# Kernel optimization log

Measured on AMD Instinct MI355X. Metric: run time of the kernel, lower is better.

## Reference

```python
import jax, jax.numpy as jnp
import numpy as np

NEG_BIG = -1e4  # matches torch masked_fill(-1e4)


def word_average(hidden, word_ids, num_words):
    """Segment-mean of token embeddings into word embeddings.
    hidden: [M, L, D], word_ids: [M, L] int in [0, num_words).
    Returns (word_reprs [M, W, D], word_mask [M, W] bool).
    Equivalent to average_by_spans: each word repr is the mean of its subword tokens;
    words with no tokens (the torch code's skipped [-1] spans) get a zero repr and mask=0.
    """
    M, L, D = hidden.shape
    seg = (jnp.arange(M, dtype=word_ids.dtype)[:, None] * num_words + word_ids).reshape(-1)
    sums = jax.ops.segment_sum(hidden.reshape(M * L, D), seg, num_segments=M * num_words)
    counts = jax.ops.segment_sum(jnp.ones((M * L,), hidden.dtype), seg, num_segments=M * num_words)
    sums = sums.reshape(M, num_words, D)
    counts = counts.reshape(M, num_words)
    mask = counts > 0
    reprs = sums / jnp.maximum(counts, 1.0)[..., None]
    return reprs, mask


def scope_pool(word_reprs, mask, proj_w, proj_b, scope_importance):
    """scope_proj_head (eval-mode dropout = identity) + scope_aware_pooling.
    word_reprs: [M, W, D], mask: [M, W]. Returns (pooled [M, D], logits [M, W, S]).
    Logits at invalid (padded) word slots are zeroed, matching torch pad_sequence padding
    applied after the projection.
    """
    logits = (jnp.einsum('mwd,ds->mws', word_reprs, proj_w) + proj_b) * mask[..., None].astype(word_reprs.dtype)
    scope_probs = jax.nn.softmax(logits, axis=-1)                      # [M, W, S]
    importance = jnp.einsum('mws,s->mw', scope_probs, scope_importance)
    importance = jnp.where(mask, importance, NEG_BIG)
    weights = jax.nn.softmax(importance, axis=-1)                      # [M, W]
    pooled = jnp.einsum('mw,mwd->md', weights, word_reprs)             # [M, D]
    return pooled, logits


def setup_inputs() -> dict:
    key = jax.random.key(0)
    ks = jax.random.split(key, 9)
    B, N, Lq, Lp, D, S = 16, 7, 256, 512, 768, 12
    Wq, Wp = 200, 400
    return {
        'q_hidden': jax.random.normal(ks[0], (B, Lq, D), jnp.float32),
        'pos_hidden': jax.random.normal(ks[1], (B, Lp, D), jnp.float32),
        'neg_hidden': jax.random.normal(ks[2], (B, N, Lp, D), jnp.float32),
        'proj_w': jax.random.normal(ks[3], (D, S), jnp.float32) * 0.02,
        'proj_b': jax.random.normal(ks[4], (S,), jnp.float32) * 0.02,
        'scope_importance': jax.random.uniform(ks[5], (S,), jnp.float32),
        'q_word_ids': jax.random.randint(ks[6], (B, Lq), 0, Wq, jnp.int32),
        'pos_word_ids': jax.random.randint(ks[7], (B, Lp), 0, Wp, jnp.int32),
        'neg_word_ids': jax.random.randint(ks[8], (B, N, Lp), 0, Wp, jnp.int32),
    }


def reference(q_hidden, pos_hidden, neg_hidden, proj_w, proj_b, scope_importance,
              q_word_ids, pos_word_ids, neg_word_ids):
    Wq = 200
    Wp = 400
    B, N, Lp, D = neg_hidden.shape

    # per-sample span averaging (ragged segment means)
    q_word, q_mask = word_average(q_hidden, q_word_ids, Wq)
    p_word, p_mask = word_average(pos_hidden, pos_word_ids, Wp)
    n_word, n_mask = word_average(neg_hidden.reshape(B * N, Lp, D),
                                  neg_word_ids.reshape(B * N, Lp), Wp)

    # scope projection + scope-aware softmax pooling
    q_pooled, q_logits = scope_pool(q_word, q_mask, proj_w, proj_b, scope_importance)
    p_pooled, p_logits = scope_pool(p_word, p_mask, proj_w, proj_b, scope_importance)
    n_pooled, _ = scope_pool(n_word, n_mask, proj_w, proj_b, scope_importance)
    n_pooled = n_pooled.reshape(B, N, D)

    return q_pooled, p_pooled, q_logits, p_logits, n_pooled
```

## Files before the change

kernel.cpp:

```cpp
#include <hip/hip_runtime.h>
#include <cfloat>

#define NEG_BIG (-1e4f)

constexpr int D = 768;
constexpr int S = 12;

constexpr int Lq = 256, Lp = 512, Wq = 200, Wp = 400;
constexpr int Mq = 16, Mp = 16, Mn = 112;

constexpr int OFF_WSUM_Q = 0;
constexpr int OFF_WSUM_P = 38400;
constexpr int OFF_WSUM_N = 115200;
constexpr int OFF_CNT_Q  = 652800;
constexpr int OFF_CNT_P  = 656000;
constexpr int OFF_CNT_N  = 662400;
constexpr int OFF_IMP_Q  = 707200;
constexpr int OFF_IMP_P  = 710400;
constexpr int OFF_IMP_N  = 716800;
constexpr int OFF_COEF   = 761600;
constexpr int WS_ZERO_FLOATS = 707200;

constexpr int OUT_QP = 0;
constexpr int OUT_PP = 12288;
constexpr int OUT_QL = 24576;
constexpr int OUT_PL = 62976;
constexpr int OUT_NP = 139776;

__global__ __launch_bounds__(192) void k_proj_accum(
    const float* __restrict__ q_h, const float* __restrict__ p_h,
    const float* __restrict__ n_h, const int* __restrict__ q_ids,
    const int* __restrict__ p_ids, const int* __restrict__ n_ids,
    const float* __restrict__ pw, float* __restrict__ ws)
{
    const int bx   = blockIdx.x;
    const int lane = threadIdx.x & 63;
    const int wv   = threadIdx.x >> 6;

    const float* h; const int* ids; float* wsum; float* cnt;
    int L, W, m, t0;
    if (bx < 128)      { h = q_h; ids = q_ids; wsum = ws + OFF_WSUM_Q; cnt = ws + OFF_CNT_Q;
                         L = Lq; W = Wq; m = bx >> 3;  t0 = (bx & 7) * 32; }
    else if (bx < 384) { int r = bx - 128;
                         h = p_h; ids = p_ids; wsum = ws + OFF_WSUM_P; cnt = ws + OFF_CNT_P;
                         L = Lp; W = Wp; m = r >> 4;  t0 = (r & 15) * 32; }
    else               { int r = bx - 384;
                         h = n_h; ids = n_ids; wsum = ws + OFF_WSUM_N; cnt = ws + OFF_CNT_N;
                         L = Lp; W = Wp; m = r >> 4;  t0 = (r & 15) * 32; }

    const int d0 = 256 * wv + 4 * lane;
    float wreg[4][S];
    {
        const float4* base = (const float4*)(pw + (size_t)d0 * S);
#pragma unroll
        for (int q = 0; q < 12; ++q) {
            float4 v = base[q];
            float tmp[4] = {v.x, v.y, v.z, v.w};
#pragma unroll
            for (int c = 0; c < 4; ++c) {
                const int li = 4 * q + c;
                wreg[li / 12][li % 12] = tmp[c];
            }
        }
    }

    const float* hbase = h + (size_t)m * L * D + d0;
    const int*   idrow = ids + m * L;

    const bool b5 = lane & 32, b4 = lane & 16, b3 = lane & 8, b2 = lane & 4;
    const int  off_s = b3 ? 2 : (b2 ? 1 : 0);
    const int  s_fin = (b5 ? 6 : 0) + (b4 ? 3 : 0) + off_s;
    const bool do_at = ((lane & 3) == 0) && !(b3 && b2);

#pragma unroll 4
    for (int t = t0; t < t0 + 32; ++t) {
        const int id = idrow[t];
        const float4 hv = *(const float4*)(hbase + (size_t)t * D);

        float p[S];
        {
            const float hj[4] = {hv.x, hv.y, hv.z, hv.w};
#pragma unroll
            for (int s = 0; s < S; ++s) p[s] = hj[0] * wreg[0][s];
#pragma unroll
            for (int j = 1; j < 4; ++j)
#pragma unroll
                for (int s = 0; s < S; ++s)
                    p[s] = fmaf(hj[j], wreg[j][s], p[s]);
        }

        float a[6];
#pragma unroll
        for (int i = 0; i < 6; ++i) {
            float snd = b5 ? p[i] : p[6 + i];
            float kp  = b5 ? p[6 + i] : p[i];
            a[i] = kp + __shfl_xor(snd, 32, 64);
        }
        float b[3];
#pragma unroll
        for (int i = 0; i < 3; ++i) {
            float snd = b4 ? a[i] : a[3 + i];
            float kp  = b4 ? a[3 + i] : a[i];
            b[i] = kp + __shfl_xor(snd, 16, 64);
        }
        float c0, c1;
        {
            float snd0 = b3 ? b[0] : b[2];
            float kp0  = b3 ? b[2] : b[0];
            c0 = kp0 + __shfl_xor(snd0, 8, 64);
            float snd1 = b3 ? b[1] : 0.f;
            float kp1  = b3 ? 0.f  : b[1];
            c1 = kp1 + __shfl_xor(snd1, 8, 64);
        }
        float snd = b3 ? c0 : (b2 ? c0 : c1);
        float kp  = b3 ? c0 : (b2 ? c1 : c0);
        float d   = kp + __shfl_xor(snd, 4, 64);
        d += __shfl_xor(d, 2, 64);
        d += __shfl_xor(d, 1, 64);

        float* wb = wsum + ((size_t)m * W + id) * S;
        if (do_at)                atomicAdd(wb + s_fin, d);
        if (wv == 0 && lane == 1) atomicAdd(cnt + (size_t)m * W + id, 1.0f);
    }
}

__global__ void k_finalize(
    const float* __restrict__ ws_c, float* __restrict__ ws_mut,
    const float* __restrict__ pb, const float* __restrict__ simp,
    float* __restrict__ out)
{
    const int idx = blockIdx.x * blockDim.x + threadIdx.x;
    if (idx >= Mq * Wq + Mp * Wp + Mn * Wp) return;

    const float* wsum; float c; float* imp; float* lgout;
    if (idx < Mq * Wq) {
        wsum = ws_c + OFF_WSUM_Q + (size_t)idx * S;  c = ws_c[OFF_CNT_Q + idx];
        imp = ws_mut + OFF_IMP_Q + idx;              lgout = out + OUT_QL + (size_t)idx * S;
    } else if (idx < Mq * Wq + Mp * Wp) {
        const int r = idx - Mq * Wq;
        wsum = ws_c + OFF_WSUM_P + (size_t)r * S;    c = ws_c[OFF_CNT_P + r];
        imp = ws_mut + OFF_IMP_P + r;                lgout = out + OUT_PL + (size_t)r * S;
    } else {
        const int r = idx - Mq * Wq - Mp * Wp;
        wsum = ws_c + OFF_WSUM_N + (size_t)r * S;    c = ws_c[OFF_CNT_N + r];
        imp = ws_mut + OFF_IMP_N + r;                lgout = nullptr;
    }

    const bool valid = (c > 0.5f);
    const float inv = valid ? 1.0f / c : 0.0f;

    float lg[S];
#pragma unroll
    for (int s = 0; s < S; ++s)
        lg[s] = valid ? (wsum[s] * inv + pb[s]) : 0.0f;

    float mx = lg[0];
#pragma unroll
    for (int s = 1; s < S; ++s) mx = fmaxf(mx, lg[s]);
    float sum = 0.f, acc = 0.f;
#pragma unroll
    for (int s = 0; s < S; ++s) {
        float e = expf(lg[s] - mx);
        sum += e;
        acc += e * simp[s];
    }
    *imp = valid ? (acc / sum) : NEG_BIG;

    if (lgout) {
#pragma unroll
        for (int s = 0; s < S; ++s) lgout[s] = lg[s];
    }
}

__global__ __launch_bounds__(256) void k_coef(
    const int* __restrict__ q_ids, const int* __restrict__ p_ids,
    const int* __restrict__ n_ids, float* __restrict__ ws)
{
    __shared__ float s_red[256];
    __shared__ float s_wgt[Wp];

    const int by  = blockIdx.x;
    const int tid = threadIdx.x;

    const int* ids; const float* impm; const float* cntm; int L, W;
    if (by < Mq)           { int m = by;
        ids = q_ids + m * Lq; impm = ws + OFF_IMP_Q + m * Wq;
        cntm = ws + OFF_CNT_Q + m * Wq; L = Lq; W = Wq; }
    else if (by < Mq + Mp) { int m = by - Mq;
        ids = p_ids + m * Lp; impm = ws + OFF_IMP_P + m * Wp;
        cntm = ws + OFF_CNT_P + m * Wp; L = Lp; W = Wp; }
    else                   { int m = by - Mq - Mp;
        ids = n_ids + m * Lp; impm = ws + OFF_IMP_N + m * Wp;
        cntm = ws + OFF_CNT_N + m * Wp; L = Lp; W = Wp; }
    float* coef = ws + OFF_COEF + (size_t)by * 512;

    float lm = -FLT_MAX;
    for (int w = tid; w < W; w += 256) lm = fmaxf(lm, impm[w]);
    s_red[tid] = lm;
    __syncthreads();
    for (int st = 128; st > 0; st >>= 1) {
        if (tid < st) s_red[tid] = fmaxf(s_red[tid], s_red[tid + st]);
        __syncthreads();
    }
    const float mx = s_red[0];
    __syncthreads();

    float ls = 0.f;
    for (int w = tid; w < W; w += 256) {
        float e = expf(impm[w] - mx);
        s_wgt[w] = e;
        ls += e;
    }
    s_red[tid] = ls;
    __syncthreads();
    for (int st = 128; st > 0; st >>= 1) {
        if (tid < st) s_red[tid] += s_red[tid + st];
        __syncthreads();
    }
    const float inv = 1.0f / s_red[0];
    for (int w = tid; w < W; w += 256) s_wgt[w] *= inv;
    __syncthreads();

    for (int l = tid; l < L; l += 256) {
        const int id = ids[l];
        coef[l] = s_wgt[id] / cntm[id];
    }
}

__global__ __launch_bounds__(192) void k_pool(
    const float* __restrict__ q_h, const float* __restrict__ p_h,
    const float* __restrict__ n_h, const float* __restrict__ ws,
    float* __restrict__ out)
{
    __shared__ float s_c[64];

    const int bx  = blockIdx.x;
    const int tid = threadIdx.x;

    const float* h; float* outp; int L, m, t0, cby;
    if (bx < 64)       { m = bx >> 2;  t0 = (bx & 3) * 64;
        h = q_h; outp = out + OUT_QP + (size_t)m * D; L = Lq; cby = m; }
    else if (bx < 192) { int r = bx - 64;  m = r >> 3;  t0 = (r & 7) * 64;
        h = p_h; outp = out + OUT_PP + (size_t)m * D; L = Lp; cby = Mq + m; }
    else               { int r = bx - 192; m = r >> 3;  t0 = (r & 7) * 64;
        h = n_h; outp = out + OUT_NP + (size_t)m * D; L = Lp; cby = Mq + Mp + m; }

    if (tid < 64) s_c[tid] = ws[OFF_COEF + (size_t)cby * 512 + t0 + tid];
    __syncthreads();

    const float* hb = h + (size_t)m * L * D + (size_t)t0 * D + 4 * tid;

    float4 acc = make_float4(0.f, 0.f, 0.f, 0.f);
#pragma unroll 8
    for (int l = 0; l < 64; ++l) {
        const float4 hv = *(const float4*)(hb + (size_t)l * D);
        const float c = s_c[l];
        acc.x = fmaf(c, hv.x, acc.x);
        acc.y = fmaf(c, hv.y, acc.y);
        acc.z = fmaf(c, hv.z, acc.z);
        acc.w = fmaf(c, hv.w, acc.w);
    }

    float* op = outp + 4 * tid;
    atomicAdd(op + 0, acc.x);
    atomicAdd(op + 1, acc.y);
    atomicAdd(op + 2, acc.z);
    atomicAdd(op + 3, acc.w);
}

extern "C" void kernel_launch(void* const* d_in, const int* in_sizes, int n_in,
                              void* d_out, int out_size, void* d_ws, size_t ws_size,
                              hipStream_t stream)
{
    const float* q_hidden   = (const float*)d_in[0];
    const float* pos_hidden = (const float*)d_in[1];
    const float* neg_hidden = (const float*)d_in[2];
    const float* proj_w     = (const float*)d_in[3];
    const float* proj_b     = (const float*)d_in[4];
    const float* simp       = (const float*)d_in[5];
    const int*   q_ids      = (const int*)d_in[6];
    const int*   p_ids      = (const int*)d_in[7];
    const int*   n_ids      = (const int*)d_in[8];
    float* out = (float*)d_out;
    float* ws  = (float*)d_ws;

    hipMemsetAsync(d_ws, 0, (size_t)WS_ZERO_FLOATS * sizeof(float), stream);
    hipMemsetAsync(out, 0, (size_t)24576 * sizeof(float), stream);
    hipMemsetAsync(out + OUT_NP, 0, (size_t)(Mn * D) * sizeof(float), stream);

    k_proj_accum<<<dim3(2176), dim3(192), 0, stream>>>(
        q_hidden, pos_hidden, neg_hidden, q_ids, p_ids, n_ids, proj_w, ws);

    k_finalize<<<dim3((Mq * Wq + Mp * Wp + Mn * Wp + 255) / 256), dim3(256), 0, stream>>>(
        ws, ws, proj_b, simp, out);

    k_coef<<<dim3(Mq + Mp + Mn), dim3(256), 0, stream>>>(q_ids, p_ids, n_ids, ws);

    k_pool<<<dim3(1088), dim3(192), 0, stream>>>(
        q_hidden, pos_hidden, neg_hidden, ws, out);
}
```

Measured before the change: 357.6 us.

## Assign one token per thread in projection kernel, drop cross-lane shuffle reduction

The projection-accumulate kernel now gives each thread one token and half of the hidden dimension (384 values), and accumulates all 12 scope logits in registers. This replaces the old mapping, in which each wave split D across lanes and needed a shuffle-tree reduction for every token. The change removes the shuffle work and issues 12 atomics per thread per token-half. In exchange, each lane reads a separate 3KB row, so global loads become strided and uncoalesced across lanes. Projection weights now come from memory (broadcast across the wave) instead of registers, and blocks shrink from 192 to 64 threads.

```diff
diff --git a/kernel.cpp b/kernel.cpp
--- a/kernel.cpp
+++ b/kernel.cpp
@@ -27,101 +27,54 @@
 constexpr int OUT_PL = 62976;
 constexpr int OUT_NP = 139776;
 
-__global__ __launch_bounds__(192) void k_proj_accum(
+__global__ __launch_bounds__(64) void k_proj_accum(
     const float* __restrict__ q_h, const float* __restrict__ p_h,
     const float* __restrict__ n_h, const int* __restrict__ q_ids,
     const int* __restrict__ p_ids, const int* __restrict__ n_ids,
     const float* __restrict__ pw, float* __restrict__ ws)
 {
     const int bx   = blockIdx.x;
-    const int lane = threadIdx.x & 63;
-    const int wv   = threadIdx.x >> 6;
+    const int lane = threadIdx.x;
 
     const float* h; const int* ids; float* wsum; float* cnt;
-    int L, W, m, t0;
+    int W, Lshift, tile, half;
     if (bx < 128)      { h = q_h; ids = q_ids; wsum = ws + OFF_WSUM_Q; cnt = ws + OFF_CNT_Q;
-                         L = Lq; W = Wq; m = bx >> 3;  t0 = (bx & 7) * 32; }
+                         W = Wq; Lshift = 8; tile = bx >> 1; half = bx & 1; }
     else if (bx < 384) { int r = bx - 128;
                          h = p_h; ids = p_ids; wsum = ws + OFF_WSUM_P; cnt = ws + OFF_CNT_P;
-                         L = Lp; W = Wp; m = r >> 4;  t0 = (r & 15) * 32; }
+                         W = Wp; Lshift = 9; tile = r >> 1; half = r & 1; }
     else               { int r = bx - 384;
                          h = n_h; ids = n_ids; wsum = ws + OFF_WSUM_N; cnt = ws + OFF_CNT_N;
-                         L = Lp; W = Wp; m = r >> 4;  t0 = (r & 15) * 32; }
-
-    const int d0 = 256 * wv + 4 * lane;
-    float wreg[4][S];
-    {
-        const float4* base = (const float4*)(pw + (size_t)d0 * S);
-#pragma unroll
-        for (int q = 0; q < 12; ++q) {
-            float4 v = base[q];
-            float tmp[4] = {v.x, v.y, v.z, v.w};
-#pragma unroll
-            for (int c = 0; c < 4; ++c) {
-                const int li = 4 * q + c;
-                wreg[li / 12][li % 12] = tmp[c];
-            }
-        }
-    }
-
-    const float* hbase = h + (size_t)m * L * D + d0;
-    const int*   idrow = ids + m * L;
-
-    const bool b5 = lane & 32, b4 = lane & 16, b3 = lane & 8, b2 = lane & 4;
-    const int  off_s = b3 ? 2 : (b2 ? 1 : 0);
-    const int  s_fin = (b5 ? 6 : 0) + (b4 ? 3 : 0) + off_s;
-    const bool do_at = ((lane & 3) == 0) && !(b3 && b2);
+                         W = Wp; Lshift = 9; tile = r >> 1; half = r & 1; }
+
+    const int flat = tile * 64 + lane;
+    const int m    = flat >> Lshift;
+    const int id   = ids[flat];
+
+    const int d0 = half * 384;
+    const float* hrow  = h + (size_t)flat * D + d0;
+    const float* wbase = pw + (size_t)d0 * S;
+
+    float p[S];
+#pragma unroll
+    for (int s = 0; s < S; ++s) p[s] = 0.f;
 
 #pragma unroll 4
-    for (int t = t0; t < t0 + 32; ++t) {
-        const int id = idrow[t];
-        const float4 hv = *(const float4*)(hbase + (size_t)t * D);
-
-        float p[S];
-        {
-            const float hj[4] = {hv.x, hv.y, hv.z, hv.w};
-#pragma unroll
-            for (int s = 0; s < S; ++s) p[s] = hj[0] * wreg[0][s];
-#pragma unroll
-            for (int j = 1; j < 4; ++j)
-#pragma unroll
-                for (int s = 0; s < S; ++s)
-                    p[s] = fmaf(hj[j], wreg[j][s], p[s]);
-        }
-
-        float a[6];
-#pragma unroll
-        for (int i = 0; i < 6; ++i) {
-            float snd = b5 ? p[i] : p[6 + i];
-            float kp  = b5 ? p[6 + i] : p[i];
-            a[i] = kp + __shfl_xor(snd, 32, 64);
-        }
-        float b[3];
-#pragma unroll
-        for (int i = 0; i < 3; ++i) {
-            float snd = b4 ? a[i] : a[3 + i];
-            float kp  = b4 ? a[3 + i] : a[i];
-            b[i] = kp + __shfl_xor(snd, 16, 64);
-        }
-        float c0, c1;
-        {
-            float snd0 = b3 ? b[0] : b[2];
-            float kp0  = b3 ? b[2] : b[0];
-            c0 = kp0 + __shfl_xor(snd0, 8, 64);
-            float snd1 = b3 ? b[1] : 0.f;
-            float kp1  = b3 ? 0.f  : b[1];
-            c1 = kp1 + __shfl_xor(snd1, 8, 64);
-        }
-        float snd = b3 ? c0 : (b2 ? c0 : c1);
-        float kp  = b3 ? c0 : (b2 ? c1 : c0);
-        float d   = kp + __shfl_xor(snd, 4, 64);
-        d += __shfl_xor(d, 2, 64);
-        d += __shfl_xor(d, 1, 64);
-
-        float* wb = wsum + ((size_t)m * W + id) * S;
-        if (do_at)                atomicAdd(wb + s_fin, d);
-        if (wv == 0 && lane == 1) atomicAdd(cnt + (size_t)m * W + id, 1.0f);
-    }
+    for (int dg = 0; dg < 96; ++dg) {
+        const float4 hv = *(const float4*)(hrow + 4 * dg);
+        const float* wr = wbase + (size_t)dg * 48;
+        const float hj[4] = {hv.x, hv.y, hv.z, hv.w};
+#pragma unroll
+        for (int j = 0; j < 4; ++j)
+#pragma unroll
+            for (int s = 0; s < S; ++s)
+                p[s] = fmaf(hj[j], wr[12 * j + s], p[s]);
+    }
+
+    float* wb = wsum + ((size_t)m * W + id) * S;
+#pragma unroll
+    for (int s = 0; s < S; ++s) atomicAdd(wb + s, p[s]);
+    if (half == 0) atomicAdd(cnt + (size_t)m * W + id, 1.0f);
 }
 
 __global__ void k_finalize(
@@ -288,7 +241,7 @@
     hipMemsetAsync(out, 0, (size_t)24576 * sizeof(float), stream);
     hipMemsetAsync(out + OUT_NP, 0, (size_t)(Mn * D) * sizeof(float), stream);
 
-    k_proj_accum<<<dim3(2176), dim3(192), 0, stream>>>(
+    k_proj_accum<<<dim3(2176), dim3(64), 0, stream>>>(
         q_hidden, pos_hidden, neg_hidden, q_ids, p_ids, n_ids, proj_w, ws);
 
     k_finalize<<<dim3((Mq * Wq + Mp * Wp + Mn * Wp + 255) / 256), dim3(256), 0, stream>>>(
```

Result: slower. 419.7 us (+17.4%).
